# Performance work log

Hardware: AMD Instinct MI355X
Metric: run time of the kernel (lower is better)

Reference implementation:

```python
import jax, jax.numpy as jnp
import numpy as np

B, H, S, D = 2, 16, 2048, 64
DILATION_RATE = 2

def dilated_global_mask(seq_len: int, dilation_rate: int) -> jnp.ndarray:
    # mask[i, j] = 1 if |i - j| % dilation_rate == 0 else 0  -> [S, S] float32
    i = jnp.arange(seq_len)[:, None]
    j = jnp.arange(seq_len)[None, :]
    return ((jnp.abs(i - j) % dilation_rate) == 0).astype(jnp.float32)

def setup_inputs() -> dict:
    key = jax.random.key(0)
    kq, kk, kv = jax.random.split(key, 3)
    queries = jax.random.normal(kq, (B, H, S, D), dtype=jnp.float32)
    keys = jax.random.normal(kk, (B, H, S, D), dtype=jnp.float32)
    values = jax.random.normal(kv, (B, H, S, D), dtype=jnp.float32)
    return {"queries": queries, "keys": keys, "values": values}

def reference(queries, keys, values):
    depth = queries.shape[-1]
    # scores: [B, H, S, S]
    scores = jnp.einsum("bhqd,bhkd->bhqk", queries, keys)
    scores = scores / jnp.sqrt(jnp.asarray(depth, dtype=jnp.float32))
    gmask = dilated_global_mask(keys.shape[-2], DILATION_RATE)  # [S, S]
    # NOTE: multiplicative masking (masked scores become 0, not -inf), as in source
    masked_scores = scores * gmask
    attention_probs = jax.nn.softmax(masked_scores, axis=-1)
    # dropout is identity at inference (training=None)
    out = jnp.einsum("bhqk,bhkd->bhqd", attention_probs, values)
    return out
```

## Files before the change

kernel.cpp:

```cpp
#include <hip/hip_runtime.h>
#include <hip/hip_bf16.h>


#define B_   2
#define H_   16
#define S_   2048
#define D_   64
#define SP_  1024
#define BQ   128
#define BK   64
#define NKT  (SP_ / BK)
#define NW   4

#define QSCALE 0.180336884f

#if __has_builtin(__builtin_amdgcn_exp2f)
#define EXP2(x) __builtin_amdgcn_exp2f(x)
#else
#define EXP2(x) exp2f(x)
#endif

typedef __bf16 bf16x8 __attribute__((ext_vector_type(8)));
typedef __bf16 bf16x4 __attribute__((ext_vector_type(4)));
typedef float  f32x4  __attribute__((ext_vector_type(4)));

#define KSW(r, c8) ((((c8) ^ ((r) & 7)) << 3))

__global__ __launch_bounds__(256, 2) void attn_kernel(const float* __restrict__ Q,
                                                      const float* __restrict__ K,
                                                      const float* __restrict__ V,
                                                      float* __restrict__ out) {
    const int bh  = blockIdx.x;
    const int par = blockIdx.y;
    const int qt  = blockIdx.z;
    const int tid  = threadIdx.x;
    const int lane = tid & 63;
    const int wave = tid >> 6;
    const int l15  = lane & 15;
    const int quad = lane >> 4;

    __shared__ __align__(16) __bf16 kbuf[2][BK][64];
    __shared__ __align__(16) __bf16 vbuf[2][D_][64];
    __shared__ __align__(16) __bf16 pt[NW][32][64];

    const size_t base = (size_t)bh * S_ * D_;
    const float* Qb = Q + base;
    const float* Kb = K + base;
    const float* Vb = V + base;
    const int vofs = (par == 0) ? D_ : -D_;

    bf16x8 qf[2][2];
    #pragma unroll
    for (int qt2 = 0; qt2 < 2; ++qt2) {
        const int qrow = qt * BQ + wave * 32 + qt2 * 16 + l15;
        const float* qsrc = Qb + (size_t)(par + 2 * qrow) * D_ + quad * 8;
        #pragma unroll
        for (int ks = 0; ks < 2; ++ks) {
            const float4 a = *(const float4*)(qsrc + ks * 32);
            const float4 b = *(const float4*)(qsrc + ks * 32 + 4);
            bf16x8 w;
            w[0] = (__bf16)(a.x * QSCALE); w[1] = (__bf16)(a.y * QSCALE);
            w[2] = (__bf16)(a.z * QSCALE); w[3] = (__bf16)(a.w * QSCALE);
            w[4] = (__bf16)(b.x * QSCALE); w[5] = (__bf16)(b.y * QSCALE);
            w[6] = (__bf16)(b.z * QSCALE); w[7] = (__bf16)(b.w * QSCALE);
            qf[qt2][ks] = w;
        }
    }

    const int kr0 = tid >> 3;
    const int kc8 = tid & 7;

    float4 pka[2], pkb[2];
    float  pv[16], pvo[16];

    auto issue_loads = [&](int kt) {
        #pragma unroll
        for (int i = 0; i < 2; ++i) {
            const int r = i * 32 + kr0;
            const float* ksrc = Kb + (size_t)(par + 2 * (kt * BK + r)) * D_ + kc8 * 8;
            pka[i] = *(const float4*)ksrc;
            pkb[i] = *(const float4*)(ksrc + 4);
        }
        #pragma unroll
        for (int i = 0; i < 2; ++i) {
            const int c = wave + 4 * i;
            const float* vsrc = Vb + (size_t)(par + 2 * (kt * BK + c * 8)) * D_ + lane;
            #pragma unroll
            for (int j = 0; j < 8; ++j) {
                pv [i * 8 + j] = vsrc[(size_t)(2 * j) * D_];
                pvo[i * 8 + j] = vsrc[(size_t)(2 * j) * D_ + vofs];
            }
        }
    };

    float vo = 0.f;
    auto stage = [&](int buf) {
        #pragma unroll
        for (int i = 0; i < 2; ++i) {
            const int r = i * 32 + kr0;
            bf16x8 w;
            w[0] = (__bf16)pka[i].x; w[1] = (__bf16)pka[i].y;
            w[2] = (__bf16)pka[i].z; w[3] = (__bf16)pka[i].w;
            w[4] = (__bf16)pkb[i].x; w[5] = (__bf16)pkb[i].y;
            w[6] = (__bf16)pkb[i].z; w[7] = (__bf16)pkb[i].w;
            *(bf16x8*)&kbuf[buf][r][KSW(r, kc8)] = w;
        }
        #pragma unroll
        for (int i = 0; i < 2; ++i) {
            const int c = wave + 4 * i;
            bf16x8 w;
            #pragma unroll
            for (int j = 0; j < 8; ++j) w[j] = (__bf16)pv[i * 8 + j];
            *(bf16x8*)&vbuf[buf][lane][KSW(lane, c)] = w;
            vo += ((pvo[i*8+0] + pvo[i*8+1]) + (pvo[i*8+2] + pvo[i*8+3]))
                + ((pvo[i*8+4] + pvo[i*8+5]) + (pvo[i*8+6] + pvo[i*8+7]));
        }
    };

    issue_loads(0);
    stage(0);
    __syncthreads();

    f32x4 acc[2][4];
    #pragma unroll
    for (int q2 = 0; q2 < 2; ++q2)
        #pragma unroll
        for (int dt = 0; dt < 4; ++dt) acc[q2][dt] = (f32x4){0.f, 0.f, 0.f, 0.f};
    float l_acc[2] = {0.f, 0.f};

    for (int kt = 0; kt < NKT; ++kt) {
        const int cur = kt & 1;
        const bool pf = (kt + 1 < NKT);

        if (pf) issue_loads(kt + 1);

        const __bf16 (*kb)[64] = kbuf[cur];
        const __bf16 (*vb)[64] = vbuf[cur];

        bf16x8 ka[2][4];
        #pragma unroll
        for (int ks = 0; ks < 2; ++ks)
            #pragma unroll
            for (int kt4 = 0; kt4 < 4; ++kt4) {
                const int R = kt4 * 16 + l15;
                ka[ks][kt4] = *(const bf16x8*)&kb[R][KSW(R, ks * 4 + quad)];
            }

        #pragma unroll
        for (int qt2 = 0; qt2 < 2; ++qt2) {
            f32x4 st[4];
            #pragma unroll
            for (int kt4 = 0; kt4 < 4; ++kt4) st[kt4] = (f32x4){0.f, 0.f, 0.f, 0.f};
            #pragma unroll
            for (int ks = 0; ks < 2; ++ks)
                #pragma unroll
                for (int kt4 = 0; kt4 < 4; ++kt4)
                    st[kt4] = __builtin_amdgcn_mfma_f32_16x16x32_bf16(
                        ka[ks][kt4], qf[qt2][ks], st[kt4], 0, 0, 0);
            #pragma unroll
            for (int kt4 = 0; kt4 < 4; ++kt4) {
                bf16x4 w;
                #pragma unroll
                for (int r = 0; r < 4; ++r) {
                    const float p = EXP2(st[kt4][r]);
                    l_acc[qt2] += p;
                    w[r] = (__bf16)p;
                }
                const int ch = (kt4 * 2 + (quad >> 1)) ^ (l15 & 7);
                *(bf16x4*)&pt[wave][qt2 * 16 + l15][ch * 8 + (quad & 1) * 4] = w;
            }
        }

        #pragma unroll
        for (int ks = 0; ks < 2; ++ks) {
            bf16x8 pa[2];
            #pragma unroll
            for (int qt2 = 0; qt2 < 2; ++qt2)
                pa[qt2] = *(const bf16x8*)
                    &pt[wave][qt2 * 16 + l15][KSW(l15, ks * 4 + quad)];
            #pragma unroll
            for (int dt = 0; dt < 4; ++dt) {
                const int Rv = dt * 16 + l15;
                const bf16x8 bv = *(const bf16x8*)&vb[Rv][KSW(Rv, ks * 4 + quad)];
                acc[0][dt] = __builtin_amdgcn_mfma_f32_16x16x32_bf16(pa[0], bv, acc[0][dt], 0, 0, 0);
                acc[1][dt] = __builtin_amdgcn_mfma_f32_16x16x32_bf16(pa[1], bv, acc[1][dt], 0, 0, 0);
            }
        }

        if (pf) stage(1 - cur);
        __syncthreads();
    }

    float* vred = (float*)pt;
    vred[wave * 64 + lane] = vo;
    __syncthreads();

    float rz[2][4];
    #pragma unroll
    for (int qt2 = 0; qt2 < 2; ++qt2) {
        float lf = l_acc[qt2];
        lf += __shfl_xor(lf, 16);
        lf += __shfl_xor(lf, 32);
        #pragma unroll
        for (int r = 0; r < 4; ++r) {
            const float lr = __shfl(lf, quad * 4 + r);
            rz[qt2][r] = 1.0f / (lr + 1024.0f);
        }
    }
    #pragma unroll
    for (int dt = 0; dt < 4; ++dt) {
        const int d = dt * 16 + l15;
        const float vso = (vred[d] + vred[64 + d]) + (vred[128 + d] + vred[192 + d]);
        #pragma unroll
        for (int qt2 = 0; qt2 < 2; ++qt2)
            #pragma unroll
            for (int r = 0; r < 4; ++r) {
                const int qg = par + 2 * (qt * BQ + wave * 32 + qt2 * 16 + quad * 4 + r);
                out[base + (size_t)qg * D_ + d] = (acc[qt2][dt][r] + vso) * rz[qt2][r];
            }
    }
}

extern "C" void kernel_launch(void* const* d_in, const int* in_sizes, int n_in,
                              void* d_out, int out_size, void* d_ws, size_t ws_size,
                              hipStream_t stream) {
    const float* Q = (const float*)d_in[0];
    const float* K = (const float*)d_in[1];
    const float* V = (const float*)d_in[2];
    float* out = (float*)d_out;
    attn_kernel<<<dim3(B_ * H_, 2, SP_ / BQ), dim3(256), 0, stream>>>(Q, K, V, out);
}
```

Measured before the change: 113.8 us.

## Feed softmax probabilities directly from registers into PV MFMA, drop P LDS round-trip

The score MFMA output layout is reused directly as the B operand of a 16x16x16 bf16 MFMA computing O^T = V^T P^T. This removes the per-wave P staging buffer in shared memory and its write/read traffic. V fragments are now loaded as bf16x4 per key-subtile. The epilogue is also reworked: outputs are transposed through LDS so each lane writes contiguous float4 rows, and per-row normalizers come straight from the transposed accumulator layout. The trade-off is twice as many smaller MFMAs and more V registers, which raises register pressure.

```diff
diff --git a/kernel.cpp b/kernel.cpp
--- a/kernel.cpp
+++ b/kernel.cpp
@@ -23,6 +23,12 @@
 typedef __bf16 bf16x8 __attribute__((ext_vector_type(8)));
 typedef __bf16 bf16x4 __attribute__((ext_vector_type(4)));
 typedef float  f32x4  __attribute__((ext_vector_type(4)));
+typedef short  s16x4  __attribute__((ext_vector_type(4)));
+
+static __device__ __forceinline__ f32x4 mfma16(bf16x4 a, bf16x4 b, f32x4 c) {
+    return __builtin_amdgcn_mfma_f32_16x16x16bf16_1k(
+        __builtin_bit_cast(s16x4, a), __builtin_bit_cast(s16x4, b), c, 0, 0, 0);
+}
 
 #define KSW(r, c8) ((((c8) ^ ((r) & 7)) << 3))
 
@@ -39,9 +45,10 @@
     const int l15  = lane & 15;
     const int quad = lane >> 4;
 
-    __shared__ __align__(16) __bf16 kbuf[2][BK][64];
-    __shared__ __align__(16) __bf16 vbuf[2][D_][64];
-    __shared__ __align__(16) __bf16 pt[NW][32][64];
+    __shared__ __align__(16) char arena[33792];
+    __bf16 (*kbuf)[BK][64] = (__bf16 (*)[BK][64])arena;
+    __bf16 (*vbuf)[D_][64] = (__bf16 (*)[D_][64])(arena + 16384);
+    float  (*vred)[64]     = (float  (*)[64])(arena + 32768);
 
     const size_t base = (size_t)bh * S_ * D_;
     const float* Qb = Q + base;
@@ -145,6 +152,17 @@
                 const int R = kt4 * 16 + l15;
                 ka[ks][kt4] = *(const bf16x8*)&kb[R][KSW(R, ks * 4 + quad)];
             }
+        bf16x4 va[4][4];
+        #pragma unroll
+        for (int dt = 0; dt < 4; ++dt) {
+            const int R = dt * 16 + l15;
+            const int ro = R & 7;
+            #pragma unroll
+            for (int kt4 = 0; kt4 < 4; ++kt4) {
+                const int ch = (kt4 * 2 + (quad >> 1)) ^ ro;
+                va[kt4][dt] = *(const bf16x4*)&vb[R][ch * 8 + (quad & 1) * 4];
+            }
+        }
 
         #pragma unroll
         for (int qt2 = 0; qt2 < 2; ++qt2) {
@@ -159,31 +177,17 @@
                         ka[ks][kt4], qf[qt2][ks], st[kt4], 0, 0, 0);
             #pragma unroll
             for (int kt4 = 0; kt4 < 4; ++kt4) {
-                bf16x4 w;
+                const float p0 = EXP2(st[kt4][0]);
+                const float p1 = EXP2(st[kt4][1]);
+                const float p2 = EXP2(st[kt4][2]);
+                const float p3 = EXP2(st[kt4][3]);
+                l_acc[qt2] += (p0 + p1) + (p2 + p3);
+                bf16x4 pb;
+                pb[0] = (__bf16)p0; pb[1] = (__bf16)p1;
+                pb[2] = (__bf16)p2; pb[3] = (__bf16)p3;
                 #pragma unroll
-                for (int r = 0; r < 4; ++r) {
-                    const float p = EXP2(st[kt4][r]);
-                    l_acc[qt2] += p;
-                    w[r] = (__bf16)p;
-                }
-                const int ch = (kt4 * 2 + (quad >> 1)) ^ (l15 & 7);
-                *(bf16x4*)&pt[wave][qt2 * 16 + l15][ch * 8 + (quad & 1) * 4] = w;
-            }
-        }
-
-        #pragma unroll
-        for (int ks = 0; ks < 2; ++ks) {
-            bf16x8 pa[2];
-            #pragma unroll
-            for (int qt2 = 0; qt2 < 2; ++qt2)
-                pa[qt2] = *(const bf16x8*)
-                    &pt[wave][qt2 * 16 + l15][KSW(l15, ks * 4 + quad)];
-            #pragma unroll
-            for (int dt = 0; dt < 4; ++dt) {
-                const int Rv = dt * 16 + l15;
-                const bf16x8 bv = *(const bf16x8*)&vb[Rv][KSW(Rv, ks * 4 + quad)];
-                acc[0][dt] = __builtin_amdgcn_mfma_f32_16x16x32_bf16(pa[0], bv, acc[0][dt], 0, 0, 0);
-                acc[1][dt] = __builtin_amdgcn_mfma_f32_16x16x32_bf16(pa[1], bv, acc[1][dt], 0, 0, 0);
+                for (int dt = 0; dt < 4; ++dt)
+                    acc[qt2][dt] = mfma16(va[kt4][dt], pb, acc[qt2][dt]);
             }
         }
 
@@ -191,33 +195,42 @@
         __syncthreads();
     }
 
-    float* vred = (float*)pt;
-    vred[wave * 64 + lane] = vo;
+    vred[wave][lane] = vo;
     __syncthreads();
 
-    float rz[2][4];
+    f32x4 vs4[4];
+    #pragma unroll
+    for (int dt = 0; dt < 4; ++dt) {
+        f32x4 s = (f32x4){0.f, 0.f, 0.f, 0.f};
+        #pragma unroll
+        for (int w = 0; w < NW; ++w)
+            s += *(const f32x4*)&vred[w][dt * 16 + quad * 4];
+        vs4[dt] = s;
+    }
+    float rz[2];
     #pragma unroll
     for (int qt2 = 0; qt2 < 2; ++qt2) {
-        float lf = l_acc[qt2];
-        lf += __shfl_xor(lf, 16);
-        lf += __shfl_xor(lf, 32);
-        #pragma unroll
-        for (int r = 0; r < 4; ++r) {
-            const float lr = __shfl(lf, quad * 4 + r);
-            rz[qt2][r] = 1.0f / (lr + 1024.0f);
-        }
-    }
-    #pragma unroll
-    for (int dt = 0; dt < 4; ++dt) {
-        const int d = dt * 16 + l15;
-        const float vso = (vred[d] + vred[64 + d]) + (vred[128 + d] + vred[192 + d]);
-        #pragma unroll
-        for (int qt2 = 0; qt2 < 2; ++qt2)
-            #pragma unroll
-            for (int r = 0; r < 4; ++r) {
-                const int qg = par + 2 * (qt * BQ + wave * 32 + qt2 * 16 + quad * 4 + r);
-                out[base + (size_t)qg * D_ + d] = (acc[qt2][dt][r] + vso) * rz[qt2][r];
-            }
+        float Z = l_acc[qt2];
+        Z += __shfl_xor(Z, 16);
+        Z += __shfl_xor(Z, 32);
+        rz[qt2] = 1.0f / (Z + 1024.0f);
+    }
+
+    float* tw = (float*)arena + wave * (16 * 68);
+    #pragma unroll
+    for (int qt2 = 0; qt2 < 2; ++qt2) {
+        #pragma unroll
+        for (int dt = 0; dt < 4; ++dt) {
+            const f32x4 o = (acc[qt2][dt] + vs4[dt]) * rz[qt2];
+            *(f32x4*)&tw[l15 * 68 + dt * 16 + quad * 4] = o;
+        }
+        #pragma unroll
+        for (int i = 0; i < 4; ++i) {
+            const int q = i * 4 + quad;
+            const f32x4 ov = *(const f32x4*)&tw[q * 68 + l15 * 4];
+            const int qg = par + 2 * (qt * BQ + wave * 32 + qt2 * 16 + q);
+            *(f32x4*)&out[base + (size_t)qg * D_ + l15 * 4] = ov;
+        }
     }
 }
 
```

New measurement: 112.2 us. Within noise of the previous version (-1.4%).
